# Optimization experiments

Measured on AMD Instinct MI355X. Metric: run time of the kernel, lower is better.

Reference implementation:

```python
import jax, jax.numpy as jnp
import numpy as np

H = 1024   # hidden_size
V = 32000  # output_size (vocab)
S = 4096   # encoder seq_len
L = 1      # n_layers


def setup_inputs() -> dict:
    key = jax.random.key(0)
    ks = jax.random.split(key, 12)
    scale = 0.02
    return {
        "word_input": jax.random.randint(ks[0], (1,), 0, V),
        "last_hidden": jax.random.normal(ks[1], (L, 1, H), jnp.float32),
        "encoder_hiddens": jax.random.normal(ks[2], (S, 1, H), jnp.float32),
        "embedding": jax.random.normal(ks[3], (V, H), jnp.float32) * scale,
        "w_ih": jax.random.normal(ks[4], (3 * H, H), jnp.float32) * scale,
        "w_hh": jax.random.normal(ks[5], (3 * H, H), jnp.float32) * scale,
        "b_ih": jax.random.normal(ks[6], (3 * H,), jnp.float32) * scale,
        "b_hh": jax.random.normal(ks[7], (3 * H,), jnp.float32) * scale,
        "attn_w": jax.random.normal(ks[8], (H, H), jnp.float32) * scale,
        "attn_b": jax.random.normal(ks[9], (H,), jnp.float32) * scale,
        "out_w": jax.random.normal(ks[10], (V, 2 * H), jnp.float32) * scale,
        "out_b": jax.random.normal(ks[11], (V,), jnp.float32) * scale,
    }


def reference(word_input, last_hidden, encoder_hiddens, embedding,
              w_ih, w_hh, b_ih, b_hh, attn_w, attn_b, out_w, out_b):
    h_dim = embedding.shape[1]
    # embedding lookup -> GRU single step (PyTorch GRU cell math)
    x = embedding[word_input[0]]            # [H]
    h0 = last_hidden[0, 0]                  # [H]
    gx = w_ih @ x + b_ih                    # [3H]
    gh = w_hh @ h0 + b_hh                   # [3H]
    r = jax.nn.sigmoid(gx[:h_dim] + gh[:h_dim])
    z = jax.nn.sigmoid(gx[h_dim:2 * h_dim] + gh[h_dim:2 * h_dim])
    n = jnp.tanh(gx[2 * h_dim:] + r * gh[2 * h_dim:])
    h = (1.0 - z) * n + z * h0              # rnn_output / new hidden [H]
    # Bahdanau-style scores: dot(hidden, attn(enc_i)) for all i, batched
    enc = encoder_hiddens[:, 0, :]          # [S, H]
    scores = (enc @ attn_w.T + attn_b) @ h  # [S]
    attn = jax.nn.softmax(scores)           # [S]
    context = attn @ enc                    # [H]
    output = jnp.concatenate([h, context]) @ out_w.T + out_b  # [V]
    return (output[None, :], h[None, None, :], attn[None, None, :])
```

## Files before the change

### kernel.cpp

```cpp
#include <hip/hip_runtime.h>
#include <cstddef>

#define Hn 1024
#define Vn 32000
#define Sn 4096

__device__ __forceinline__ float wave_reduce_sum(float v) {
#pragma unroll
    for (int o = 32; o > 0; o >>= 1) v += __shfl_down(v, o, 64);
    return v;
}


__global__ __launch_bounds__(256) void k_gru(const int* __restrict__ word,
                                             const float* __restrict__ emb,
                                             const float* __restrict__ h0,
                                             const float* __restrict__ w_ih,
                                             const float* __restrict__ w_hh,
                                             const float* __restrict__ b_ih,
                                             const float* __restrict__ b_hh,
                                             float* __restrict__ ws_h,
                                             float* __restrict__ out_h)
{
    const int k = blockIdx.x;
    const int t = threadIdx.x;
    const float* x = emb + (size_t)word[0] * Hn;
    const float4 xv = ((const float4*)x)[t];
    const float4 hv = ((const float4*)h0)[t];

    float acc[6];
    const float* rows[6] = {
        w_ih + (size_t)k * Hn, w_ih + (size_t)(k + Hn) * Hn, w_ih + (size_t)(k + 2 * Hn) * Hn,
        w_hh + (size_t)k * Hn, w_hh + (size_t)(k + Hn) * Hn, w_hh + (size_t)(k + 2 * Hn) * Hn
    };
#pragma unroll
    for (int g = 0; g < 6; ++g) {
        const float4 w = ((const float4*)rows[g])[t];
        const float4 vv = (g < 3) ? xv : hv;
        acc[g] = w.x * vv.x + w.y * vv.y + w.z * vv.z + w.w * vv.w;
    }

    __shared__ float red[6][4];
    const int wv = t >> 6, lane = t & 63;
#pragma unroll
    for (int g = 0; g < 6; ++g) {
        const float s = wave_reduce_sum(acc[g]);
        if (lane == 0) red[g][wv] = s;
    }
    __syncthreads();
    if (t == 0) {
        float g0 = red[0][0] + red[0][1] + red[0][2] + red[0][3] + b_ih[k];
        float g1 = red[1][0] + red[1][1] + red[1][2] + red[1][3] + b_ih[k + Hn];
        float g2 = red[2][0] + red[2][1] + red[2][2] + red[2][3] + b_ih[k + 2 * Hn];
        float g3 = red[3][0] + red[3][1] + red[3][2] + red[3][3] + b_hh[k];
        float g4 = red[4][0] + red[4][1] + red[4][2] + red[4][3] + b_hh[k + Hn];
        float g5 = red[5][0] + red[5][1] + red[5][2] + red[5][3] + b_hh[k + 2 * Hn];
        float r = 1.f / (1.f + expf(-(g0 + g3)));
        float z = 1.f / (1.f + expf(-(g1 + g4)));
        float n = tanhf(g2 + r * g5);
        float hk = (1.f - z) * n + z * h0[k];
        ws_h[k]  = hk;
        out_h[k] = hk;
    }
}

__global__ __launch_bounds__(256) void k_attnv(const float* __restrict__ attn_w,
                                               const float* __restrict__ ws_h,
                                               float* __restrict__ v)
{
    const int t = threadIdx.x;
    const int tj = t >> 4;
    const int tk = t & 15;
    const int k = blockIdx.x * 16 + tk;
    float acc = 0.f;
    for (int j = tj; j < Hn; j += 16)
        acc += attn_w[(size_t)j * Hn + k] * ws_h[j];
    __shared__ float p[16][17];
    p[tj][tk] = acc;
    __syncthreads();
    if (t < 16) {
        float s = 0.f;
#pragma unroll
        for (int j = 0; j < 16; ++j) s += p[j][t];
        v[blockIdx.x * 16 + t] = s;
    }
}

__global__ __launch_bounds__(256) void k_scores(const float* __restrict__ enc,
                                                const float* __restrict__ ws_v,
                                                float* __restrict__ scores)
{
    __shared__ float v[Hn];
    const int t = threadIdx.x;
    ((float4*)v)[t] = ((const float4*)ws_v)[t];
    __syncthreads();
    const int wv = t >> 6, lane = t & 63;
    const int s = blockIdx.x * 4 + wv;
    const float* row = enc + (size_t)s * Hn;
    float acc = 0.f;
#pragma unroll
    for (int k = 0; k < 4; ++k) {
        const int idx = k * 256 + lane * 4;
        const float4 e = *(const float4*)(row + idx);
        acc += e.x * v[idx] + e.y * v[idx + 1] + e.z * v[idx + 2] + e.w * v[idx + 3];
    }
    acc = wave_reduce_sum(acc);
    if (lane == 0) scores[s] = acc;
}

__global__ __launch_bounds__(1024) void k_softmax(const float* __restrict__ scores,
                                                  float* __restrict__ attn_ws,
                                                  float* __restrict__ attn_out)
{
    const int t = threadIdx.x;
    const float4 sc = ((const float4*)scores)[t];
    __shared__ float red[16];
    __shared__ float bval;
    const int wv = t >> 6, lane = t & 63;

    float m = fmaxf(fmaxf(sc.x, sc.y), fmaxf(sc.z, sc.w));
#pragma unroll
    for (int o = 32; o > 0; o >>= 1) m = fmaxf(m, __shfl_down(m, o, 64));
    if (lane == 0) red[wv] = m;
    __syncthreads();
    if (t == 0) {
        float mm = red[0];
        for (int i = 1; i < 16; ++i) mm = fmaxf(mm, red[i]);
        bval = mm;
    }
    __syncthreads();
    const float mx = bval;
    const float e0 = expf(sc.x - mx), e1 = expf(sc.y - mx);
    const float e2 = expf(sc.z - mx), e3 = expf(sc.w - mx);
    const float ps = wave_reduce_sum(e0 + e1 + e2 + e3);
    __syncthreads();
    if (lane == 0) red[wv] = ps;
    __syncthreads();
    if (t == 0) {
        float s = 0.f;
        for (int i = 0; i < 16; ++i) s += red[i];
        bval = 1.f / s;
    }
    __syncthreads();
    const float inv = bval;
    const float4 o4 = make_float4(e0 * inv, e1 * inv, e2 * inv, e3 * inv);
    ((float4*)attn_ws)[t]  = o4;
    ((float4*)attn_out)[t] = o4;
}

__global__ __launch_bounds__(256) void k_ctx_part(const float* __restrict__ enc,
                                                  const float* __restrict__ attn,
                                                  float* __restrict__ partial)
{
    const int jc = blockIdx.x & 3;
    const int sc = blockIdx.x >> 2;
    const int j = jc * 256 + threadIdx.x;
    float acc = 0.f;
    const int s0 = sc * 128;
    for (int s = s0; s < s0 + 128; ++s)
        acc += attn[s] * enc[(size_t)s * Hn + j];
    partial[(size_t)sc * Hn + j] = acc;
}

__global__ __launch_bounds__(256) void k_ctx_red(const float* __restrict__ partial,
                                                 float* __restrict__ ctx)
{
    const int j = blockIdx.x * 256 + threadIdx.x;
    float acc = 0.f;
#pragma unroll
    for (int sc = 0; sc < 32; ++sc) acc += partial[(size_t)sc * Hn + j];
    ctx[j] = acc;
}

__global__ __launch_bounds__(256) void k_out(const float* __restrict__ out_w,
                                             const float* __restrict__ out_b,
                                             const float* __restrict__ c2,
                                             float* __restrict__ out)
{
    __shared__ float c[2 * Hn];
    const int t = threadIdx.x;
    ((float4*)c)[t]       = ((const float4*)c2)[t];
    ((float4*)c)[t + 256] = ((const float4*)c2)[t + 256];
    __syncthreads();
    const int wv = t >> 6, lane = t & 63;
    const int row = blockIdx.x * 4 + wv;
    const float* w = out_w + (size_t)row * (2 * Hn);
    float acc = 0.f;
#pragma unroll
    for (int k = 0; k < 8; ++k) {
        const int idx = k * 256 + lane * 4;
        const float4 wv4 = *(const float4*)(w + idx);
        acc += wv4.x * c[idx] + wv4.y * c[idx + 1] + wv4.z * c[idx + 2] + wv4.w * c[idx + 3];
    }
    acc = wave_reduce_sum(acc);
    if (lane == 0) out[row] = acc + out_b[row];
}

extern "C" void kernel_launch(void* const* d_in, const int* in_sizes, int n_in,
                              void* d_out, int out_size, void* d_ws, size_t ws_size,
                              hipStream_t stream) {
    const int*   word   = (const int*)d_in[0];
    const float* h_last = (const float*)d_in[1];
    const float* enc    = (const float*)d_in[2];
    const float* emb    = (const float*)d_in[3];
    const float* w_ih   = (const float*)d_in[4];
    const float* w_hh   = (const float*)d_in[5];
    const float* b_ih   = (const float*)d_in[6];
    const float* b_hh   = (const float*)d_in[7];
    const float* attn_w = (const float*)d_in[8];
    const float* out_w  = (const float*)d_in[10];
    const float* out_b  = (const float*)d_in[11];
    float* out = (float*)d_out;
    float* ws  = (float*)d_ws;

    float* ws_h      = ws;
    float* ws_ctx    = ws + 1024;
    float* ws_v      = ws + 2048;
    float* ws_scores = ws + 3072;
    float* ws_attn   = ws + 7168;
    float* ws_part   = ws + 11264;

    k_gru<<<Hn, 256, 0, stream>>>(word, emb, h_last, w_ih, w_hh, b_ih, b_hh, ws_h, out + Vn);
    k_attnv<<<Hn / 16, 256, 0, stream>>>(attn_w, ws_h, ws_v);
    k_scores<<<Sn / 4, 256, 0, stream>>>(enc, ws_v, ws_scores);
    k_softmax<<<1, 1024, 0, stream>>>(ws_scores, ws_attn, out + Vn + Hn);
    k_ctx_part<<<128, 256, 0, stream>>>(enc, ws_attn, ws_part);
    k_ctx_red<<<4, 256, 0, stream>>>(ws_part, ws_ctx);
    k_out<<<Vn / 4, 256, 0, stream>>>(out_w, out_b, ws, out);
}
```

Baseline: 86.62 us.

## Fuse GRU, attention, softmax and context into one cooperative grid-synced kernel

Six small kernels (GRU, attn vector, scores, softmax, context partials, context reduce) are replaced by one cooperative kernel of 256 blocks that uses grid.sync between phases. This removes several kernel launch gaps and the single-block softmax kernel, since each block now recomputes the softmax max and sum redundantly and applies exp on the fly inside the context loop. The trade-off is grid-wide barrier cost, fewer blocks per phase (GRU now one wave per row, ctx partials 64 per block), and the 64-way partial reduction.

Measured after the change: 198.4 us. +129.0%, slower.

```diff
diff --git a/kernel.cpp b/kernel.cpp
--- a/kernel.cpp
+++ b/kernel.cpp
@@ -1,5 +1,8 @@
 #include <hip/hip_runtime.h>
+#include <hip/hip_cooperative_groups.h>
 #include <cstddef>
+
+namespace cg = cooperative_groups;
 
 #define Hn 1024
 #define Vn 32000
@@ -10,166 +13,158 @@
     for (int o = 32; o > 0; o >>= 1) v += __shfl_down(v, o, 64);
     return v;
 }
-
-
-__global__ __launch_bounds__(256) void k_gru(const int* __restrict__ word,
-                                             const float* __restrict__ emb,
-                                             const float* __restrict__ h0,
-                                             const float* __restrict__ w_ih,
-                                             const float* __restrict__ w_hh,
-                                             const float* __restrict__ b_ih,
-                                             const float* __restrict__ b_hh,
-                                             float* __restrict__ ws_h,
-                                             float* __restrict__ out_h)
+__device__ __forceinline__ float wave_reduce_max(float v) {
+#pragma unroll
+    for (int o = 32; o > 0; o >>= 1) v = fmaxf(v, __shfl_down(v, o, 64));
+    return v;
+}
+
+
+__global__ __launch_bounds__(256) void k_fused(const int* __restrict__ word,
+                                               const float* __restrict__ emb,
+                                               const float* __restrict__ h0,
+                                               const float* __restrict__ w_ih,
+                                               const float* __restrict__ w_hh,
+                                               const float* __restrict__ b_ih,
+                                               const float* __restrict__ b_hh,
+                                               const float* __restrict__ attn_w,
+                                               const float* __restrict__ enc,
+                                               float* __restrict__ ws_h,
+                                               float* __restrict__ ws_v,
+                                               float* __restrict__ ws_scores,
+                                               float* __restrict__ ws_part,
+                                               float* __restrict__ ws_ctx,
+                                               float* __restrict__ out_h,
+                                               float* __restrict__ out_attn)
 {
-    const int k = blockIdx.x;
-    const int t = threadIdx.x;
-    const float* x = emb + (size_t)word[0] * Hn;
-    const float4 xv = ((const float4*)x)[t];
-    const float4 hv = ((const float4*)h0)[t];
-
-    float acc[6];
-    const float* rows[6] = {
-        w_ih + (size_t)k * Hn, w_ih + (size_t)(k + Hn) * Hn, w_ih + (size_t)(k + 2 * Hn) * Hn,
-        w_hh + (size_t)k * Hn, w_hh + (size_t)(k + Hn) * Hn, w_hh + (size_t)(k + 2 * Hn) * Hn
-    };
-#pragma unroll
-    for (int g = 0; g < 6; ++g) {
-        const float4 w = ((const float4*)rows[g])[t];
-        const float4 vv = (g < 3) ? xv : hv;
-        acc[g] = w.x * vv.x + w.y * vv.y + w.z * vv.z + w.w * vv.w;
-    }
-
-    __shared__ float red[6][4];
+    cg::grid_group grid = cg::this_grid();
+    const int t = threadIdx.x, bid = blockIdx.x;
     const int wv = t >> 6, lane = t & 63;
-#pragma unroll
-    for (int g = 0; g < 6; ++g) {
-        const float s = wave_reduce_sum(acc[g]);
-        if (lane == 0) red[g][wv] = s;
-    }
-    __syncthreads();
-    if (t == 0) {
-        float g0 = red[0][0] + red[0][1] + red[0][2] + red[0][3] + b_ih[k];
-        float g1 = red[1][0] + red[1][1] + red[1][2] + red[1][3] + b_ih[k + Hn];
-        float g2 = red[2][0] + red[2][1] + red[2][2] + red[2][3] + b_ih[k + 2 * Hn];
-        float g3 = red[3][0] + red[3][1] + red[3][2] + red[3][3] + b_hh[k];
-        float g4 = red[4][0] + red[4][1] + red[4][2] + red[4][3] + b_hh[k + Hn];
-        float g5 = red[5][0] + red[5][1] + red[5][2] + red[5][3] + b_hh[k + 2 * Hn];
-        float r = 1.f / (1.f + expf(-(g0 + g3)));
-        float z = 1.f / (1.f + expf(-(g1 + g4)));
-        float n = tanhf(g2 + r * g5);
-        float hk = (1.f - z) * n + z * h0[k];
-        ws_h[k]  = hk;
-        out_h[k] = hk;
-    }
-}
-
-__global__ __launch_bounds__(256) void k_attnv(const float* __restrict__ attn_w,
-                                               const float* __restrict__ ws_h,
-                                               float* __restrict__ v)
-{
-    const int t = threadIdx.x;
-    const int tj = t >> 4;
-    const int tk = t & 15;
-    const int k = blockIdx.x * 16 + tk;
-    float acc = 0.f;
-    for (int j = tj; j < Hn; j += 16)
-        acc += attn_w[(size_t)j * Hn + k] * ws_h[j];
-    __shared__ float p[16][17];
-    p[tj][tk] = acc;
-    __syncthreads();
-    if (t < 16) {
-        float s = 0.f;
-#pragma unroll
-        for (int j = 0; j < 16; ++j) s += p[j][t];
-        v[blockIdx.x * 16 + t] = s;
-    }
-}
-
-__global__ __launch_bounds__(256) void k_scores(const float* __restrict__ enc,
-                                                const float* __restrict__ ws_v,
-                                                float* __restrict__ scores)
-{
-    __shared__ float v[Hn];
-    const int t = threadIdx.x;
-    ((float4*)v)[t] = ((const float4*)ws_v)[t];
-    __syncthreads();
-    const int wv = t >> 6, lane = t & 63;
-    const int s = blockIdx.x * 4 + wv;
-    const float* row = enc + (size_t)s * Hn;
-    float acc = 0.f;
-#pragma unroll
-    for (int k = 0; k < 4; ++k) {
-        const int idx = k * 256 + lane * 4;
-        const float4 e = *(const float4*)(row + idx);
-        acc += e.x * v[idx] + e.y * v[idx + 1] + e.z * v[idx + 2] + e.w * v[idx + 3];
-    }
-    acc = wave_reduce_sum(acc);
-    if (lane == 0) scores[s] = acc;
-}
-
-__global__ __launch_bounds__(1024) void k_softmax(const float* __restrict__ scores,
-                                                  float* __restrict__ attn_ws,
-                                                  float* __restrict__ attn_out)
-{
-    const int t = threadIdx.x;
-    const float4 sc = ((const float4*)scores)[t];
-    __shared__ float red[16];
-    __shared__ float bval;
-    const int wv = t >> 6, lane = t & 63;
-
-    float m = fmaxf(fmaxf(sc.x, sc.y), fmaxf(sc.z, sc.w));
-#pragma unroll
-    for (int o = 32; o > 0; o >>= 1) m = fmaxf(m, __shfl_down(m, o, 64));
-    if (lane == 0) red[wv] = m;
-    __syncthreads();
-    if (t == 0) {
-        float mm = red[0];
-        for (int i = 1; i < 16; ++i) mm = fmaxf(mm, red[i]);
-        bval = mm;
-    }
-    __syncthreads();
-    const float mx = bval;
-    const float e0 = expf(sc.x - mx), e1 = expf(sc.y - mx);
-    const float e2 = expf(sc.z - mx), e3 = expf(sc.w - mx);
-    const float ps = wave_reduce_sum(e0 + e1 + e2 + e3);
-    __syncthreads();
-    if (lane == 0) red[wv] = ps;
-    __syncthreads();
-    if (t == 0) {
-        float s = 0.f;
-        for (int i = 0; i < 16; ++i) s += red[i];
-        bval = 1.f / s;
-    }
-    __syncthreads();
-    const float inv = bval;
-    const float4 o4 = make_float4(e0 * inv, e1 * inv, e2 * inv, e3 * inv);
-    ((float4*)attn_ws)[t]  = o4;
-    ((float4*)attn_out)[t] = o4;
-}
-
-__global__ __launch_bounds__(256) void k_ctx_part(const float* __restrict__ enc,
-                                                  const float* __restrict__ attn,
-                                                  float* __restrict__ partial)
-{
-    const int jc = blockIdx.x & 3;
-    const int sc = blockIdx.x >> 2;
-    const int j = jc * 256 + threadIdx.x;
-    float acc = 0.f;
-    const int s0 = sc * 128;
-    for (int s = s0; s < s0 + 128; ++s)
-        acc += attn[s] * enc[(size_t)s * Hn + j];
-    partial[(size_t)sc * Hn + j] = acc;
-}
-
-__global__ __launch_bounds__(256) void k_ctx_red(const float* __restrict__ partial,
-                                                 float* __restrict__ ctx)
-{
-    const int j = blockIdx.x * 256 + threadIdx.x;
-    float acc = 0.f;
-#pragma unroll
-    for (int sc = 0; sc < 32; ++sc) acc += partial[(size_t)sc * Hn + j];
-    ctx[j] = acc;
+    __shared__ float smem[1024];
+
+    {
+        const int k = bid * 4 + wv;
+        const float* x = emb + (size_t)word[0] * Hn;
+        float4 xv[4], hv[4];
+#pragma unroll
+        for (int i = 0; i < 4; ++i) {
+            const int idx = i * 256 + lane * 4;
+            xv[i] = *(const float4*)(x + idx);
+            hv[i] = *(const float4*)(h0 + idx);
+        }
+        const float* rowp[6] = {
+            w_ih + (size_t)k * Hn, w_ih + (size_t)(k + Hn) * Hn, w_ih + (size_t)(k + 2 * Hn) * Hn,
+            w_hh + (size_t)k * Hn, w_hh + (size_t)(k + Hn) * Hn, w_hh + (size_t)(k + 2 * Hn) * Hn
+        };
+        float acc[6];
+#pragma unroll
+        for (int g = 0; g < 6; ++g) {
+            float a = 0.f;
+#pragma unroll
+            for (int i = 0; i < 4; ++i) {
+                const int idx = i * 256 + lane * 4;
+                const float4 w4 = *(const float4*)(rowp[g] + idx);
+                const float4 vv = (g < 3) ? xv[i] : hv[i];
+                a += w4.x * vv.x + w4.y * vv.y + w4.z * vv.z + w4.w * vv.w;
+            }
+            acc[g] = wave_reduce_sum(a);
+        }
+        if (lane == 0) {
+            const float g0 = acc[0] + b_ih[k], g1 = acc[1] + b_ih[k + Hn], g2 = acc[2] + b_ih[k + 2 * Hn];
+            const float g3 = acc[3] + b_hh[k], g4 = acc[4] + b_hh[k + Hn], g5 = acc[5] + b_hh[k + 2 * Hn];
+            const float r = 1.f / (1.f + expf(-(g0 + g3)));
+            const float z = 1.f / (1.f + expf(-(g1 + g4)));
+            const float n = tanhf(g2 + r * g5);
+            const float hk = (1.f - z) * n + z * h0[k];
+            ws_h[k]  = hk;
+            out_h[k] = hk;
+        }
+    }
+    grid.sync();
+
+    if (bid < 64) {
+        const int tj = t >> 4, tk = t & 15;
+        const int k = bid * 16 + tk;
+        float acc = 0.f;
+        for (int j = tj; j < Hn; j += 16)
+            acc += attn_w[(size_t)j * Hn + k] * ws_h[j];
+        smem[tj * 17 + tk] = acc;
+        __syncthreads();
+        if (t < 16) {
+            float s = 0.f;
+#pragma unroll
+            for (int j = 0; j < 16; ++j) s += smem[j * 17 + t];
+            ws_v[bid * 16 + t] = s;
+        }
+    }
+    grid.sync();
+
+    {
+        ((float4*)smem)[t] = ((const float4*)ws_v)[t];
+        __syncthreads();
+#pragma unroll
+        for (int q = 0; q < 4; ++q) {
+            const int s = bid * 16 + wv * 4 + q;
+            const float* row = enc + (size_t)s * Hn;
+            float a = 0.f;
+#pragma unroll
+            for (int i = 0; i < 4; ++i) {
+                const int idx = i * 256 + lane * 4;
+                const float4 e = *(const float4*)(row + idx);
+                a += e.x * smem[idx] + e.y * smem[idx + 1] + e.z * smem[idx + 2] + e.w * smem[idx + 3];
+            }
+            a = wave_reduce_sum(a);
+            if (lane == 0) ws_scores[s] = a;
+        }
+    }
+    grid.sync();
+
+    float mx, inv;
+    {
+        float4 sc[4];
+#pragma unroll
+        for (int i = 0; i < 4; ++i) sc[i] = ((const float4*)ws_scores)[i * 256 + t];
+        float m = -1e30f;
+#pragma unroll
+        for (int i = 0; i < 4; ++i)
+            m = fmaxf(m, fmaxf(fmaxf(sc[i].x, sc[i].y), fmaxf(sc[i].z, sc[i].w)));
+        m = wave_reduce_max(m);
+        if (lane == 0) smem[wv] = m;
+        __syncthreads();
+        mx = fmaxf(fmaxf(smem[0], smem[1]), fmaxf(smem[2], smem[3]));
+        float ps = 0.f;
+#pragma unroll
+        for (int i = 0; i < 4; ++i)
+            ps += expf(sc[i].x - mx) + expf(sc[i].y - mx) + expf(sc[i].z - mx) + expf(sc[i].w - mx);
+        ps = wave_reduce_sum(ps);
+        __syncthreads();
+        if (lane == 0) smem[wv] = ps;
+        __syncthreads();
+        inv = 1.f / (smem[0] + smem[1] + smem[2] + smem[3]);
+    }
+
+    {
+        const int jc = bid & 3, sc = bid >> 2;
+        const int j = jc * 256 + t;
+        const int s0 = sc * 64;
+        float acc = 0.f;
+        for (int s = s0; s < s0 + 64; ++s) {
+            const float a = expf(ws_scores[s] - mx) * inv;
+            acc += a * enc[(size_t)s * Hn + j];
+        }
+        ws_part[(size_t)sc * Hn + j] = acc;
+        if (jc == 0 && t < 64)
+            out_attn[s0 + t] = expf(ws_scores[s0 + t] - mx) * inv;
+    }
+    grid.sync();
+
+    if (bid < 4) {
+        const int j = bid * 256 + t;
+        float acc = 0.f;
+#pragma unroll
+        for (int sc2 = 0; sc2 < 64; ++sc2) acc += ws_part[(size_t)sc2 * Hn + j];
+        ws_ctx[j] = acc;
+    }
 }
 
 __global__ __launch_bounds__(256) void k_out(const float* __restrict__ out_w,
@@ -189,8 +184,8 @@
 #pragma unroll
     for (int k = 0; k < 8; ++k) {
         const int idx = k * 256 + lane * 4;
-        const float4 wv4 = *(const float4*)(w + idx);
-        acc += wv4.x * c[idx] + wv4.y * c[idx + 1] + wv4.z * c[idx + 2] + wv4.w * c[idx + 3];
+        const float4 w4 = *(const float4*)(w + idx);
+        acc += w4.x * c[idx] + w4.y * c[idx + 1] + w4.z * c[idx + 2] + w4.w * c[idx + 3];
     }
     acc = wave_reduce_sum(acc);
     if (lane == 0) out[row] = acc + out_b[row];
@@ -217,14 +212,16 @@
     float* ws_ctx    = ws + 1024;
     float* ws_v      = ws + 2048;
     float* ws_scores = ws + 3072;
-    float* ws_attn   = ws + 7168;
-    float* ws_part   = ws + 11264;
-
-    k_gru<<<Hn, 256, 0, stream>>>(word, emb, h_last, w_ih, w_hh, b_ih, b_hh, ws_h, out + Vn);
-    k_attnv<<<Hn / 16, 256, 0, stream>>>(attn_w, ws_h, ws_v);
-    k_scores<<<Sn / 4, 256, 0, stream>>>(enc, ws_v, ws_scores);
-    k_softmax<<<1, 1024, 0, stream>>>(ws_scores, ws_attn, out + Vn + Hn);
-    k_ctx_part<<<128, 256, 0, stream>>>(enc, ws_attn, ws_part);
-    k_ctx_red<<<4, 256, 0, stream>>>(ws_part, ws_ctx);
+    float* ws_part   = ws + 7168;
+    float* out_h     = out + Vn;
+    float* out_attn  = out + Vn + Hn;
+
+    void* args[] = {
+        (void*)&word, (void*)&emb, (void*)&h_last, (void*)&w_ih, (void*)&w_hh,
+        (void*)&b_ih, (void*)&b_hh, (void*)&attn_w, (void*)&enc,
+        (void*)&ws_h, (void*)&ws_v, (void*)&ws_scores, (void*)&ws_part, (void*)&ws_ctx,
+        (void*)&out_h, (void*)&out_attn
+    };
+    hipLaunchCooperativeKernel((void*)k_fused, dim3(256), dim3(256), args, 0, stream);
     k_out<<<Vn / 4, 256, 0, stream>>>(out_w, out_b, ws, out);
 }
```

## Fuse softmax and context reduction into one kernel with atomic accumulation

Applied to the files above, without the earlier changes.

Replaces the single-block softmax, partial-context and reduction kernels with one kernel. Each block recomputes the global max and sum from all scores, normalises its own 64-score slice, and accumulates its weighted encoder rows into the context vector with atomicAdd. The context buffer is zeroed inside the GRU kernel. This removes two launches and the serial single-block softmax step, at the cost of every block redundantly reading all 4096 scores, a non-deterministic float atomic summation order, and 64 blocks that may underuse the GPU.

Result: no change. 86.19 us (-0.5%).

```diff
diff --git a/kernel.cpp b/kernel.cpp
--- a/kernel.cpp
+++ b/kernel.cpp
@@ -8,6 +8,11 @@
 __device__ __forceinline__ float wave_reduce_sum(float v) {
 #pragma unroll
     for (int o = 32; o > 0; o >>= 1) v += __shfl_down(v, o, 64);
+    return v;
+}
+__device__ __forceinline__ float wave_reduce_max(float v) {
+#pragma unroll
+    for (int o = 32; o > 0; o >>= 1) v = fmaxf(v, __shfl_down(v, o, 64));
     return v;
 }
 
@@ -20,10 +25,17 @@
                                              const float* __restrict__ b_ih,
                                              const float* __restrict__ b_hh,
                                              float* __restrict__ ws_h,
+                                             float* __restrict__ ws_ctx,
                                              float* __restrict__ out_h)
 {
     const int k = blockIdx.x;
     const int t = threadIdx.x;
+
+    if (k == 0) {
+#pragma unroll
+        for (int i = 0; i < 4; ++i) ws_ctx[t + i * 256] = 0.f;
+    }
+
     const float* x = emb + (size_t)word[0] * Hn;
     const float4 xv = ((const float4*)x)[t];
     const float4 hv = ((const float4*)h0)[t];
@@ -108,68 +120,60 @@
     if (lane == 0) scores[s] = acc;
 }
 
-__global__ __launch_bounds__(1024) void k_softmax(const float* __restrict__ scores,
-                                                  float* __restrict__ attn_ws,
-                                                  float* __restrict__ attn_out)
-{
-    const int t = threadIdx.x;
-    const float4 sc = ((const float4*)scores)[t];
-    __shared__ float red[16];
-    __shared__ float bval;
-    const int wv = t >> 6, lane = t & 63;
-
-    float m = fmaxf(fmaxf(sc.x, sc.y), fmaxf(sc.z, sc.w));
-#pragma unroll
-    for (int o = 32; o > 0; o >>= 1) m = fmaxf(m, __shfl_down(m, o, 64));
+__global__ __launch_bounds__(256) void k_ctx(const float* __restrict__ enc,
+                                             const float* __restrict__ scores,
+                                             float* __restrict__ ctx,
+                                             float* __restrict__ out_attn)
+{
+    const int t = threadIdx.x, bid = blockIdx.x;
+    const int wv = t >> 6, lane = t & 63;
+    __shared__ float red[4];
+    __shared__ float aw[64];
+
+    float4 sc[4];
+#pragma unroll
+    for (int i = 0; i < 4; ++i) sc[i] = ((const float4*)scores)[i * 256 + t];
+    float m = -1e30f;
+#pragma unroll
+    for (int i = 0; i < 4; ++i)
+        m = fmaxf(m, fmaxf(fmaxf(sc[i].x, sc[i].y), fmaxf(sc[i].z, sc[i].w)));
+    m = wave_reduce_max(m);
     if (lane == 0) red[wv] = m;
     __syncthreads();
-    if (t == 0) {
-        float mm = red[0];
-        for (int i = 1; i < 16; ++i) mm = fmaxf(mm, red[i]);
-        bval = mm;
-    }
-    __syncthreads();
-    const float mx = bval;
-    const float e0 = expf(sc.x - mx), e1 = expf(sc.y - mx);
-    const float e2 = expf(sc.z - mx), e3 = expf(sc.w - mx);
-    const float ps = wave_reduce_sum(e0 + e1 + e2 + e3);
+    const float mx = fmaxf(fmaxf(red[0], red[1]), fmaxf(red[2], red[3]));
+    float ps = 0.f;
+#pragma unroll
+    for (int i = 0; i < 4; ++i)
+        ps += expf(sc[i].x - mx) + expf(sc[i].y - mx) + expf(sc[i].z - mx) + expf(sc[i].w - mx);
+    ps = wave_reduce_sum(ps);
     __syncthreads();
     if (lane == 0) red[wv] = ps;
     __syncthreads();
-    if (t == 0) {
-        float s = 0.f;
-        for (int i = 0; i < 16; ++i) s += red[i];
-        bval = 1.f / s;
-    }
-    __syncthreads();
-    const float inv = bval;
-    const float4 o4 = make_float4(e0 * inv, e1 * inv, e2 * inv, e3 * inv);
-    ((float4*)attn_ws)[t]  = o4;
-    ((float4*)attn_out)[t] = o4;
-}
-
-__global__ __launch_bounds__(256) void k_ctx_part(const float* __restrict__ enc,
-                                                  const float* __restrict__ attn,
-                                                  float* __restrict__ partial)
-{
-    const int jc = blockIdx.x & 3;
-    const int sc = blockIdx.x >> 2;
-    const int j = jc * 256 + threadIdx.x;
-    float acc = 0.f;
-    const int s0 = sc * 128;
-    for (int s = s0; s < s0 + 128; ++s)
-        acc += attn[s] * enc[(size_t)s * Hn + j];
-    partial[(size_t)sc * Hn + j] = acc;
-}
-
-__global__ __launch_bounds__(256) void k_ctx_red(const float* __restrict__ partial,
-                                                 float* __restrict__ ctx)
-{
-    const int j = blockIdx.x * 256 + threadIdx.x;
-    float acc = 0.f;
-#pragma unroll
-    for (int sc = 0; sc < 32; ++sc) acc += partial[(size_t)sc * Hn + j];
-    ctx[j] = acc;
+    const float inv = 1.f / (red[0] + red[1] + red[2] + red[3]);
+
+    const int s0 = bid * 64;
+    if (t < 64) {
+        const float a = expf(scores[s0 + t] - mx) * inv;
+        aw[t] = a;
+        out_attn[s0 + t] = a;
+    }
+    __syncthreads();
+
+    float acc0 = 0.f, acc1 = 0.f, acc2 = 0.f, acc3 = 0.f;
+    const float* base = enc + (size_t)s0 * Hn;
+#pragma unroll 4
+    for (int s = 0; s < 64; ++s) {
+        const float a = aw[s];
+        const float* row = base + (size_t)s * Hn;
+        acc0 += a * row[t];
+        acc1 += a * row[t + 256];
+        acc2 += a * row[t + 512];
+        acc3 += a * row[t + 768];
+    }
+    atomicAdd(&ctx[t],       acc0);
+    atomicAdd(&ctx[t + 256], acc1);
+    atomicAdd(&ctx[t + 512], acc2);
+    atomicAdd(&ctx[t + 768], acc3);
 }
 
 __global__ __launch_bounds__(256) void k_out(const float* __restrict__ out_w,
@@ -189,8 +193,8 @@
 #pragma unroll
     for (int k = 0; k < 8; ++k) {
         const int idx = k * 256 + lane * 4;
-        const float4 wv4 = *(const float4*)(w + idx);
-        acc += wv4.x * c[idx] + wv4.y * c[idx + 1] + wv4.z * c[idx + 2] + wv4.w * c[idx + 3];
+        const float4 w4 = *(const float4*)(w + idx);
+        acc += w4.x * c[idx] + w4.y * c[idx + 1] + w4.z * c[idx + 2] + w4.w * c[idx + 3];
     }
     acc = wave_reduce_sum(acc);
     if (lane == 0) out[row] = acc + out_b[row];
@@ -217,14 +221,10 @@
     float* ws_ctx    = ws + 1024;
     float* ws_v      = ws + 2048;
     float* ws_scores = ws + 3072;
-    float* ws_attn   = ws + 7168;
-    float* ws_part   = ws + 11264;
-
-    k_gru<<<Hn, 256, 0, stream>>>(word, emb, h_last, w_ih, w_hh, b_ih, b_hh, ws_h, out + Vn);
+
+    k_gru<<<Hn, 256, 0, stream>>>(word, emb, h_last, w_ih, w_hh, b_ih, b_hh, ws_h, ws_ctx, out + Vn);
     k_attnv<<<Hn / 16, 256, 0, stream>>>(attn_w, ws_h, ws_v);
     k_scores<<<Sn / 4, 256, 0, stream>>>(enc, ws_v, ws_scores);
-    k_softmax<<<1, 1024, 0, stream>>>(ws_scores, ws_attn, out + Vn + Hn);
-    k_ctx_part<<<128, 256, 0, stream>>>(enc, ws_attn, ws_part);
-    k_ctx_red<<<4, 256, 0, stream>>>(ws_part, ws_ctx);
+    k_ctx<<<Sn / 64, 256, 0, stream>>>(enc, ws_scores, ws_ctx, out + Vn + Hn);
     k_out<<<Vn / 4, 256, 0, stream>>>(out_w, out_b, ws, out);
 }
```
